# Performance work log

Hardware: AMD Instinct MI355X
Metric: run time of the kernel (lower is better)

Reference implementation:

```python
import jax, jax.numpy as jnp
import numpy as np

TAU = 0.05       # sinkhorn temperature (functools.partial in GCN_Net)
SK_ITERS = 20    # sinkhorn max_iter


def _mlp(x, w1, b1, w2, b2):
    # nn.Sequential(Linear, ReLU, Linear)
    return jnp.maximum(x @ w1 + b1, 0.0) @ w2 + b2


def _cosine(f1, f2, eps=1e-8):
    # torch CosineSimilarity over broadcast (E1,1,D) x (1,E2,D), computed as a GEMM
    n1 = jnp.maximum(jnp.linalg.norm(f1, axis=-1), eps)
    n2 = jnp.maximum(jnp.linalg.norm(f2, axis=-1), eps)
    return (f1 @ f2.T) / (n1[:, None] * n2[None, :])


def _sinkhorn(s):
    # log-domain sinkhorn, alternating row/col normalization (pygmtools-style)
    log_s = s / TAU
    for i in range(SK_ITERS):
        log_s = log_s - jax.nn.logsumexp(log_s, axis=(1 if i % 2 == 0 else 0), keepdims=True)
    return jnp.exp(log_s)


def _build_conn_edges(preds):
    # fully-connected off-diagonal graph; edge feats [dx, dy, dist, cls_src, cls_dst]
    n = preds.shape[0]
    pos = preds[:, 1:3]
    cls = preds[:, 6]
    idx = np.arange(n)
    r, c = np.meshgrid(idx, idx, indexing='ij')
    m = r != c
    conn = np.stack([r[m], c[m]], axis=1)  # (E,2), static under jit
    src, dst = conn[:, 0], conn[:, 1]
    d = pos[dst] - pos[src]                             # (E,2)
    dist = jnp.linalg.norm(d, axis=-1, keepdims=True)   # (E,1)
    edges = jnp.concatenate([d, dist, cls[src][:, None], cls[dst][:, None]], axis=-1)  # (E,5)
    return jnp.asarray(conn), edges


def _forward(ego_preds, cav_preds, node_w1, node_b1, node_w2, node_b2,
             edge_w1, edge_b1, edge_w2, edge_b2,
             l0_self_w, l0_self_b, l0_conv_w, l0_conv_b, l0_cls_w, l0_cls_b,
             l1_self_w, l1_self_b, l1_conv_w, l1_conv_b, l1_cls_w, l1_cls_b,
             fc_w, fc_b):
    ego = ego_preds[0]
    cav = cav_preds[0]
    n1, n2 = ego.shape[0], cav.shape[0]
    conn1, e1 = _build_conn_edges(ego)
    conn2, e2 = _build_conn_edges(cav)
    # --- NodeMLP affinity ---
    f1 = _mlp(ego[:, 1:6], node_w1, node_b1, node_w2, node_b2)
    f2 = _mlp(cav[:, 1:6], node_w1, node_b1, node_w2, node_b2)
    cls_eq = (ego[:, 6][:, None] == cav[:, 6][None, :]).astype(ego.dtype)
    conf = jnp.sum(jnp.sqrt(ego[:, 7:][:, None, :] * cav[:, 7:][None, :, :]), axis=-1)
    node_aff = cls_eq * conf * _cosine(f1, f2)                         # (n1,n2)
    # --- EdgeMLP affinity ---
    g1 = _mlp(e1[:, :3], edge_w1, edge_b1, edge_w2, edge_b2)
    g2 = _mlp(e2[:, :3], edge_w1, edge_b1, edge_w2, edge_b2)
    ecls = jnp.all(e1[:, 3:].astype(jnp.int32)[:, None, :] == e2[:, 3:].astype(jnp.int32)[None, :, :],
                   axis=-1).astype(ego.dtype)
    edge_aff = ecls * _cosine(g1, g2)                                  # (E1,E2)
    # --- Lawler affinity matrix K over association graph: node (i,a) -> i*n2+a ---
    N = n1 * n2
    rows = (conn1[:, 0][:, None] * n2 + conn2[:, 0][None, :]).ravel()
    cols = (conn1[:, 1][:, None] * n2 + conn2[:, 1][None, :]).ravel()
    K = jnp.zeros((N, N), ego.dtype).at[rows, cols].set(edge_aff.ravel())
    d_idx = jnp.arange(N)
    K = K.at[d_idx, d_idx].set(node_aff.ravel())
    # --- GCN adjacency = nonzero pattern of K, with added self-loops + sym norm ---
    A = (K != 0).astype(ego.dtype) + jnp.eye(N, dtype=ego.dtype)
    dinv = jax.lax.rsqrt(A.sum(axis=1))
    normA = dinv[:, None] * A * dinv[None, :]
    x = jnp.diag(K)[:, None]                                           # (N,1)
    # --- NGMConvLayers: self-loop Linear + GCNConv + sinkhorn channel ---
    for sw, sb, cw, cb, kw, kb in (
            (l0_self_w, l0_self_b, l0_conv_w, l0_conv_b, l0_cls_w, l0_cls_b),
            (l1_self_w, l1_self_b, l1_conv_w, l1_conv_b, l1_cls_w, l1_cls_b)):
        x = (x @ sw + sb) + (normA @ (x @ cw) + cb)
        sk = _sinkhorn((x @ kw + kb).reshape(n1, n2))
        x = x + sk.reshape(-1, 1)
    scores = x @ fc_w + fc_b                                           # (N,1)
    s = scores.reshape(n2, n1).T                                       # view(n2,-1).t()
    return _sinkhorn(s)


def setup_inputs() -> dict:
    key = jax.random.key(0)
    ks = jax.random.split(key, 16)

    def lin(k, fi, fo):
        kw, kb = jax.random.split(k)
        s = (2.0 / (fi + fo)) ** 0.5
        return (jax.random.normal(kw, (fi, fo), jnp.float32) * s,
                jax.random.normal(kb, (fo,), jnp.float32) * 0.01)

    def make_preds(k, n):
        k1, k2 = jax.random.split(k)
        p = jax.random.uniform(k1, (1, n, 8), jnp.float32)
        cls = jnp.floor(jax.random.uniform(k2, (1, n)) * 3.0)  # 3 discrete classes
        p = p.at[:, :, 6].set(cls)
        p = p.at[:, :, 7].set(0.1 + 0.9 * p[:, :, 7])          # positive confidences
        return p

    inp = {'ego_preds': make_preds(ks[0], 64), 'cav_preds': make_preds(ks[1], 64)}
    inp['node_w1'], inp['node_b1'] = lin(ks[2], 5, 64)
    inp['node_w2'], inp['node_b2'] = lin(ks[3], 64, 32)
    inp['edge_w1'], inp['edge_b1'] = lin(ks[4], 3, 64)
    inp['edge_w2'], inp['edge_b2'] = lin(ks[5], 64, 32)
    inp['l0_self_w'], inp['l0_self_b'] = lin(ks[6], 1, 16)
    inp['l0_conv_w'], inp['l0_conv_b'] = lin(ks[7], 1, 16)
    inp['l0_cls_w'], inp['l0_cls_b'] = lin(ks[8], 16, 1)
    inp['l1_self_w'], inp['l1_self_b'] = lin(ks[9], 16, 16)
    inp['l1_conv_w'], inp['l1_conv_b'] = lin(ks[10], 16, 16)
    inp['l1_cls_w'], inp['l1_cls_b'] = lin(ks[11], 16, 1)
    inp['fc_w'], inp['fc_b'] = lin(ks[12], 16, 1)
    return inp


def reference(ego_preds, cav_preds, node_w1, node_b1, node_w2, node_b2,
              edge_w1, edge_b1, edge_w2, edge_b2,
              l0_self_w, l0_self_b, l0_conv_w, l0_conv_b, l0_cls_w, l0_cls_b,
              l1_self_w, l1_self_b, l1_conv_w, l1_conv_b, l1_cls_w, l1_cls_b,
              fc_w, fc_b):
    return _forward(ego_preds, cav_preds, node_w1, node_b1, node_w2, node_b2,
                    edge_w1, edge_b1, edge_w2, edge_b2,
                    l0_self_w, l0_self_b, l0_conv_w, l0_conv_b, l0_cls_w, l0_cls_b,
                    l1_self_w, l1_self_b, l1_conv_w, l1_conv_b, l1_cls_w, l1_cls_b,
                    fc_w, fc_b)
```

## Files before the change

### kernel.cpp

```cpp
#include <hip/hip_runtime.h>
#include <math.h>


#define SK_SCALE 28.853900817779268f

template<int CTRL>
__device__ __forceinline__ float dppf(float x) {
    int xi = __float_as_int(x);
    int rr = __builtin_amdgcn_update_dpp(xi, xi, CTRL, 0xF, 0xF, false);
    return __int_as_float(rr);
}
__device__ __forceinline__ float red16_max(float v) {
    v = fmaxf(v, dppf<0xB1>(v));
    v = fmaxf(v, dppf<0x4E>(v));
    v = fmaxf(v, dppf<0x141>(v));
    v = fmaxf(v, dppf<0x140>(v));
    return v;
}
__device__ __forceinline__ float red16_sum(float v) {
    v += dppf<0xB1>(v); v += dppf<0x4E>(v); v += dppf<0x141>(v); v += dppf<0x140>(v);
    return v;
}
__device__ __forceinline__ float e2f(float x) { return __builtin_amdgcn_exp2f(x); }
__device__ __forceinline__ float rcpf(float x) { return __builtin_amdgcn_rcpf(x); }
__device__ __forceinline__ float dot4(const float4 a, const float4 b) {
    return a.x*b.x + a.y*b.y + a.z*b.z + a.w*b.w;
}
__device__ __forceinline__ void fma4(float4& a, float b, const float4 c) {
    a.x += b*c.x; a.y += b*c.y; a.z += b*c.z; a.w += b*c.w;
}
__device__ __forceinline__ void add4(float4& a, const float4 c) {
    a.x += c.x; a.y += c.y; a.z += c.z; a.w += c.w;
}
__device__ __forceinline__ void ld4(const float* p, float* o) {
    float4 v = *(const float4*)p; o[0]=v.x; o[1]=v.y; o[2]=v.z; o[3]=v.w;
}

__device__ void sk_mult(const float* tq, const float* tt, int s, int pr,
                        float* up, float* vp, float* rmp,
                        float* aq, float* att, float* u_out, float* v_out) {
    float rm = red16_max(fmaxf(fmaxf(tq[0], tq[1]), fmaxf(tq[2], tq[3])));
    #pragma unroll
    for (int k = 0; k < 4; ++k) aq[k] = e2f(tq[k] - rm);
    float u = rcpf(red16_sum(aq[0] + aq[1] + aq[2] + aq[3]));
    if (s == 0) { rmp[pr] = rm; up[pr] = u; }
    __syncthreads();
    float rmq[4]; ld4(rmp + 4*s, rmq);
    #pragma unroll
    for (int k = 0; k < 4; ++k) att[k] = e2f(tt[k] - rmq[k]);
    float v;
    {
        float uq[4]; ld4(up + 4*s, uq);
        v = rcpf(red16_sum(att[0]*uq[0] + att[1]*uq[1] + att[2]*uq[2] + att[3]*uq[3]));
        if (s == 0) vp[pr] = v;
        __syncthreads();
    }
    #pragma unroll 1
    for (int p = 0; p < 9; ++p) {
        float vq[4]; ld4(vp + 4*s, vq);
        u = rcpf(red16_sum(aq[0]*vq[0] + aq[1]*vq[1] + aq[2]*vq[2] + aq[3]*vq[3]));
        if (s == 0) up[pr] = u;
        __syncthreads();
        float uq[4]; ld4(up + 4*s, uq);
        v = rcpf(red16_sum(att[0]*uq[0] + att[1]*uq[1] + att[2]*uq[2] + att[3]*uq[3]));
        if (s == 0) vp[pr] = v;
        __syncthreads();
    }
    *u_out = u; *v_out = v;
}

__device__ void matvec_dual(const float* u1, const float* u1t, const float* u2, const float* u2t,
                            const float* mmq, const float* dqv, const float* mmt, const float* dqt,
                            float* o1, float* o1t, float* o2, float* o2t,
                            int s, int pr,
                            float* WR1p, float* WC1p, float* WR2p, float* WC2p) {
    float z1[4], z2[4], z1t[4], z2t[4];
    float rs1 = 0, rs2 = 0, cs1 = 0, cs2 = 0;
    #pragma unroll
    for (int k = 0; k < 4; ++k) {
        float md = mmq[k] * dqv[k], mdt = mmt[k] * dqt[k];
        z1[k] = md * u1[k];   z2[k] = md * u2[k];
        z1t[k] = mdt * u1t[k]; z2t[k] = mdt * u2t[k];
        rs1 += z1[k]; rs2 += z2[k]; cs1 += z1t[k]; cs2 += z2t[k];
    }
    rs1 = red16_sum(rs1); rs2 = red16_sum(rs2);
    cs1 = red16_sum(cs1); cs2 = red16_sum(cs2);
    if (s == 0) { WR1p[pr] = rs1; WR2p[pr] = rs2; WC1p[pr] = cs1; WC2p[pr] = cs2; }
    __syncthreads();
    float wr1[4], wc1[4], wr2[4], wc2[4];
    ld4(WR1p + 4*s, wr1); ld4(WC1p + 4*s, wc1);
    ld4(WR2p + 4*s, wr2); ld4(WC2p + 4*s, wc2);
    float W1 = red16_sum(wc1[0] + wc1[1] + wc1[2] + wc1[3]);
    float W2 = red16_sum(wc2[0] + wc2[1] + wc2[2] + wc2[3]);
    #pragma unroll
    for (int k = 0; k < 4; ++k) {
        float d = dqv[k], mm = mmq[k], dt = dqt[k], mt = mmt[k];
        o1[k]  = d  * ((1.0f + mm) * d  * u1[k]  + mm * (W1 - rs1 - wc1[k] + z1[k]));
        o2[k]  = d  * ((1.0f + mm) * d  * u2[k]  + mm * (W2 - rs2 - wc2[k] + z2[k]));
        o1t[k] = dt * ((1.0f + mt) * dt * u1t[k] + mt * (W1 - wr1[k] - cs1 + z1t[k]));
        o2t[k] = dt * ((1.0f + mt) * dt * u2t[k] + mt * (W2 - wr2[k] - cs2 + z2t[k]));
    }
}

extern "C" __global__ __launch_bounds__(1024)
void gcn_match_kernel(const float* ego, const float* cav,
                      const float* nw1, const float* nb1, const float* nw2, const float* nb2,
                      const float* sw0, const float* sb0, const float* cw0, const float* cb0,
                      const float* kw0, const float* kb0,
                      const float* sw1, const float* sb1, const float* cw1, const float* cb1,
                      const float* kw1, const float* kb1,
                      const float* fcw, const float* fcb,
                      float* out) {
    __shared__ __align__(16) float sh_hT1[64 * 68];
    __shared__ __align__(16) float sh_hT2[64 * 68];
    __shared__ __align__(16) float sh_w2[2048];
    __shared__ __align__(16) float sh_f1[64 * 36];
    __shared__ __align__(16) float sh_f2[64 * 36];
    __shared__ __align__(16) float sh_nb2[32];
    __shared__ float sh_cls1[64], sh_cf1[64], sh_n1[64];
    __shared__ __align__(16) float sh_cls1p[64], sh_cf1p[64], sh_n1p[64];
    __shared__ __align__(16) float sh_cls2p[64], sh_cf2p[64], sh_n2p[64];
    __shared__ __align__(16) float sh_Drp[64], sh_Dcp[64];
    __shared__ __align__(16) float sh_rmp[64], sh_up[64], sh_vp[64];
    __shared__ __align__(16) float sh_WR1p[64], sh_WC1p[64], sh_WR2p[64], sh_WC2p[64];
    __shared__ float sh_avec[7 * 16];
    __shared__ float sh_coef[18];

    const int tid  = threadIdx.x;
    const int wave = tid >> 6, lane = tid & 63;
    const int r = tid >> 4, s = tid & 15;
    const int pr = 4 * (r & 15) + (r >> 4);
    float* sh_dots = sh_hT1;

    if (tid < 512) ((float4*)sh_w2)[tid] = ((const float4*)nw2)[tid];
    if (tid < 32) sh_nb2[tid] = nb2[tid];
    if (tid < 64) {
        float c = ego[tid * 8 + 6], f = ego[tid * 8 + 7];
        int p = 4 * (tid & 15) + (tid >> 4);
        sh_cls1[tid] = c; sh_cf1[tid] = f; sh_cls1p[p] = c; sh_cf1p[p] = f;
    } else if (tid < 128) {
        int j = tid - 64, p = 4 * (j & 15) + (j >> 4);
        sh_cls2p[p] = cav[j * 8 + 6]; sh_cf2p[p] = cav[j * 8 + 7];
    }
    {
        const float* X = (wave < 8) ? ego : cav;
        float* HT = (wave < 8) ? sh_hT1 : sh_hT2;
        const int k0 = (wave & 7) * 8;
        float4 xa = ((const float4*)X)[lane * 2];
        float4 xb = ((const float4*)X)[lane * 2 + 1];
        #pragma unroll
        for (int kk = 0; kk < 8; ++kk) {
            int k = k0 + kk;
            float acc = nb1[k] + xa.y * nw1[k] + xa.z * nw1[64 + k] + xa.w * nw1[128 + k]
                      + xb.x * nw1[192 + k] + xb.y * nw1[256 + k];
            HT[k * 68 + lane] = fmaxf(acc, 0.0f);
        }
    }
    __syncthreads();

    if (wave < 2) {
        const float* HT = (wave == 0) ? sh_hT1 : sh_hT2;
        float* F = (wave == 0) ? sh_f1 : sh_f2;
        const int rr = lane >> 2, oq = lane & 3;
        float4 accA[4], accB[4];
        #pragma unroll
        for (int m = 0; m < 4; ++m) { accA[m] = make_float4(0,0,0,0); accB[m] = accA[m]; }
        #pragma unroll 4
        for (int k = 0; k < 64; ++k) {
            float4 hq = *(const float4*)(HT + k * 68 + 4 * rr);
            float4 wA = *(const float4*)(sh_w2 + k * 32 + 4 * oq);
            float4 wB = *(const float4*)(sh_w2 + k * 32 + 16 + 4 * oq);
            fma4(accA[0], hq.x, wA); fma4(accB[0], hq.x, wB);
            fma4(accA[1], hq.y, wA); fma4(accB[1], hq.y, wB);
            fma4(accA[2], hq.z, wA); fma4(accB[2], hq.z, wB);
            fma4(accA[3], hq.w, wA); fma4(accB[3], hq.w, wB);
        }
        float4 b2a = *(const float4*)(sh_nb2 + 4 * oq);
        float4 b2b = *(const float4*)(sh_nb2 + 16 + 4 * oq);
        float sq[4];
        #pragma unroll
        for (int m = 0; m < 4; ++m) {
            add4(accA[m], b2a); add4(accB[m], b2b);
            int row = 4 * rr + m;
            *(float4*)(F + row * 36 + 4 * oq)      = accA[m];
            *(float4*)(F + row * 36 + 16 + 4 * oq) = accB[m];
            float q = dot4(accA[m], accA[m]) + dot4(accB[m], accB[m]);
            q += dppf<0xB1>(q); q += dppf<0x4E>(q);
            sq[m] = q;
        }
        if (oq == 0) {
            #pragma unroll
            for (int m = 0; m < 4; ++m) {
                int row = 4 * rr + m, p = 4 * (row & 15) + (row >> 4);
                float n = fmaxf(sqrtf(sq[m]), 1e-8f);
                if (wave == 0) { sh_n1[row] = n; sh_n1p[p] = n; }
                else           { sh_n2p[p] = n; }
            }
        }
    } else if (wave == 2 && lane < 16) {
        int o = lane;
        float ax = 0, av = 0, as_ = 0, aw = 0, au = 0, ae = 0, a1 = 0;
        for (int k = 0; k < 16; ++k) {
            float s0k = sw0[k], c0k = cw0[k], b0k = sb0[k] + cb0[k];
            float s1ko = sw1[k * 16 + o], c1ko = cw1[k * 16 + o];
            ax += s0k * s1ko;  av += c0k * s1ko + s0k * c1ko;  as_ += s1ko;
            aw += c0k * c1ko;  au += c1ko;  ae += b0k * c1ko;  a1 += b0k * s1ko;
        }
        a1 += sb1[o] + cb1[o];
        sh_avec[0*16+o] = ax; sh_avec[1*16+o] = av; sh_avec[2*16+o] = as_;
        sh_avec[3*16+o] = aw; sh_avec[4*16+o] = au; sh_avec[5*16+o] = ae;
        sh_avec[6*16+o] = a1;
    }
    __syncthreads();

    if (wave < 4) {
        const int sc = lane & 15, rc = lane >> 4;
        float dt[4][4];
        #pragma unroll
        for (int m = 0; m < 4; ++m)
            #pragma unroll
            for (int k = 0; k < 4; ++k) dt[m][k] = 0.0f;
        for (int kq = 0; kq < 8; ++kq) {
            float4 f2q[4];
            #pragma unroll
            for (int k = 0; k < 4; ++k)
                f2q[k] = *(const float4*)(sh_f2 + (sc + 16 * k) * 36 + 4 * kq);
            #pragma unroll
            for (int m = 0; m < 4; ++m) {
                int rrow = 16 * m + 4 * wave + rc;
                float4 f1q = *(const float4*)(sh_f1 + rrow * 36 + 4 * kq);
                #pragma unroll
                for (int k = 0; k < 4; ++k) dt[m][k] += dot4(f1q, f2q[k]);
            }
        }
        #pragma unroll
        for (int m = 0; m < 4; ++m) {
            int rrow = 16 * m + 4 * wave + rc;
            *(float4*)(sh_dots + rrow * 68 + 4 * sc) =
                make_float4(dt[m][0], dt[m][1], dt[m][2], dt[m][3]);
        }
    } else if (wave == 4 && lane < 18) {
        int t = lane; float c = 0.0f;
        if (t == 0)      { for (int k = 0; k < 16; ++k) c += sw0[k] * kw0[k]; }
        else if (t == 1) { for (int k = 0; k < 16; ++k) c += cw0[k] * kw0[k]; }
        else if (t == 2) { for (int k = 0; k < 16; ++k) c += (sb0[k] + cb0[k]) * kw0[k]; c += kb0[0]; }
        else if (t < 10) { int v = t - 3;
            for (int o = 0; o < 16; ++o) c += sh_avec[v * 16 + o] * kw1[o];
            if (v == 6) c += kb1[0];
        } else if (t < 17) { int v = t - 10;
            for (int o = 0; o < 16; ++o) c += sh_avec[v * 16 + o] * fcw[o];
            if (v == 6) c += fcb[0];
        } else { for (int o = 0; o < 16; ++o) c += fcw[o]; }
        sh_coef[t] = c;
    }
    float mmq[4], mmt[4], cfq[4], cft[4];
    float Drr, Dcr;
    {
        const float cls1r = sh_cls1[r], cls2r = sh_cls2p[pr];
        const float cf1r = sh_cf1[r],  cf2r  = sh_cf2p[pr];
        float c2q[4], c1q[4], f2q[4], f1q[4];
        ld4(sh_cls2p + 4*s, c2q); ld4(sh_cls1p + 4*s, c1q);
        ld4(sh_cf2p + 4*s, f2q);  ld4(sh_cf1p + 4*s, f1q);
        float dr = 0, dc = 0;
        #pragma unroll
        for (int k = 0; k < 4; ++k) {
            mmq[k] = (cls1r == c2q[k]) ? 1.0f : 0.0f;
            mmt[k] = (c1q[k] == cls2r) ? 1.0f : 0.0f;
            dr += mmq[k]; dc += mmt[k];
            cfq[k] = sqrtf(cf1r * f2q[k]);
            cft[k] = sqrtf(f1q[k] * cf2r);
        }
        Drr = red16_sum(dr);
        Dcr = red16_sum(dc);
        if (s == 0) { sh_Drp[pr] = Drr; sh_Dcp[pr] = Dcr; }
    }
    __syncthreads();

    float dqv[4], dqt[4], x0[4], x0t[4];
    {
        float dcq[4], drq[4], n2q[4], n1q[4], dotq[4];
        ld4(sh_Dcp + 4*s, dcq); ld4(sh_Drp + 4*s, drq);
        ld4(sh_n2p + 4*s, n2q); ld4(sh_n1p + 4*s, n1q);
        ld4(sh_dots + r * 68 + 4*s, dotq);
        float Tdeg = red16_sum(dcq[0] + dcq[1] + dcq[2] + dcq[3]);
        const float n1r = sh_n1[r], n2r = sh_n2p[pr];
        #pragma unroll
        for (int k = 0; k < 4; ++k) {
            dqv[k] = (mmq[k] != 0.0f) ? (1.0f / sqrtf(Tdeg - Drr - dcq[k] + 3.0f)) : 1.0f;
            dqt[k] = (mmt[k] != 0.0f) ? (1.0f / sqrtf(Tdeg - drq[k] - Dcr + 3.0f)) : 1.0f;
            x0[k] = mmq[k] * cfq[k] * (dotq[k] / (n1r * n2q[k]));
            float dott = sh_dots[(s + 16 * k) * 68 + pr];
            x0t[k] = mmt[k] * cft[k] * (dott / (n1q[k] * n2r));
        }
    }

    float v0[4], v0t[4], oe[4], oet[4];
    {
        float ones[4] = {1.0f, 1.0f, 1.0f, 1.0f};
        matvec_dual(x0, x0t, ones, ones, mmq, dqv, mmt, dqt,
                    v0, v0t, oe, oet, s, pr, sh_WR1p, sh_WC1p, sh_WR2p, sh_WC2p);
    }

    float aq[4], att[4], u0, vv0;
    float s0[4], s0t[4];
    {
        float c0 = sh_coef[0], c1 = sh_coef[1], c2 = sh_coef[2];
        float t0q[4], t0t[4];
        #pragma unroll
        for (int k = 0; k < 4; ++k) {
            t0q[k] = (c0 * x0[k]  + c1 * v0[k]  + c2) * SK_SCALE;
            t0t[k] = (c0 * x0t[k] + c1 * v0t[k] + c2) * SK_SCALE;
        }
        sk_mult(t0q, t0t, s, pr, sh_up, sh_vp, sh_rmp, aq, att, &u0, &vv0);
        float vq[4], uq[4];
        ld4(sh_vp + 4*s, vq); ld4(sh_up + 4*s, uq);
        #pragma unroll
        for (int k = 0; k < 4; ++k) {
            s0[k]  = aq[k] * u0 * vq[k];
            s0t[k] = att[k] * uq[k] * vv0;
        }
    }

    float ov[4], ovt[4], os[4], ost[4];
    matvec_dual(v0, v0t, s0, s0t, mmq, dqv, mmt, dqt,
                ov, ovt, os, ost, s, pr, sh_WR1p, sh_WC1p, sh_WR2p, sh_WC2p);
    float t1q[4], t1t[4], sacc[4], sacct[4];
    {
        float ctx = sh_coef[3], ctv = sh_coef[4], cts = sh_coef[5];
        float cw_ = sh_coef[6], cu_ = sh_coef[7], ce_ = sh_coef[8], ct1 = sh_coef[9];
        float csx = sh_coef[10], csv = sh_coef[11], css = sh_coef[12];
        float cw2 = sh_coef[13], cu2 = sh_coef[14], ce2 = sh_coef[15], cs1 = sh_coef[16];
        #pragma unroll
        for (int k = 0; k < 4; ++k) {
            t1q[k] = (ctx * x0[k] + ctv * v0[k] + cts * s0[k] + ct1
                    + cw_ * ov[k] + cu_ * os[k] + ce_ * oe[k]) * SK_SCALE;
            t1t[k] = (ctx * x0t[k] + ctv * v0t[k] + cts * s0t[k] + ct1
                    + cw_ * ovt[k] + cu_ * ost[k] + ce_ * oet[k]) * SK_SCALE;
            sacc[k] = csx * x0[k] + csv * v0[k] + css * s0[k] + cs1
                    + cw2 * ov[k] + cu2 * os[k] + ce2 * oe[k];
            sacct[k] = csx * x0t[k] + csv * v0t[k] + css * s0t[k] + cs1
                    + cw2 * ovt[k] + cu2 * ost[k] + ce2 * oet[k];
        }
    }

    {
        float u1, v1;
        sk_mult(t1q, t1t, s, pr, sh_up, sh_vp, sh_rmp, aq, att, &u1, &v1);
        float c17 = sh_coef[17];
        float vq[4], uq[4];
        ld4(sh_vp + 4*s, vq); ld4(sh_up + 4*s, uq);
        #pragma unroll
        for (int k = 0; k < 4; ++k) {
            sacc[k]  += c17 * aq[k] * u1 * vq[k];
            sacct[k] += c17 * att[k] * uq[k] * v1;
        }
    }
    __syncthreads();

    {
        float t2q[4], t2t[4];
        #pragma unroll
        for (int k = 0; k < 4; ++k) {
            t2q[k] = sacct[k] * SK_SCALE;
            t2t[k] = sacc[k] * SK_SCALE;
        }
        float u2, v2;
        sk_mult(t2q, t2t, s, pr, sh_up, sh_vp, sh_rmp, aq, att, &u2, &v2);
        float vq[4]; ld4(sh_vp + 4*s, vq);
        #pragma unroll
        for (int k = 0; k < 4; ++k)
            out[(r << 6) + s + (k << 4)] = aq[k] * u2 * vq[k];
    }
}

extern "C" void kernel_launch(void* const* d_in, const int* in_sizes, int n_in,
                              void* d_out, int out_size, void* d_ws, size_t ws_size,
                              hipStream_t stream) {
    const float* ego = (const float*)d_in[0];
    const float* cav = (const float*)d_in[1];
    const float* nw1 = (const float*)d_in[2];
    const float* nb1 = (const float*)d_in[3];
    const float* nw2 = (const float*)d_in[4];
    const float* nb2 = (const float*)d_in[5];
    const float* sw0 = (const float*)d_in[10];
    const float* sb0 = (const float*)d_in[11];
    const float* cw0 = (const float*)d_in[12];
    const float* cb0 = (const float*)d_in[13];
    const float* kw0 = (const float*)d_in[14];
    const float* kb0 = (const float*)d_in[15];
    const float* sw1 = (const float*)d_in[16];
    const float* sb1 = (const float*)d_in[17];
    const float* cw1 = (const float*)d_in[18];
    const float* cb1 = (const float*)d_in[19];
    const float* kw1 = (const float*)d_in[20];
    const float* kb1 = (const float*)d_in[21];
    const float* fcw = (const float*)d_in[22];
    const float* fcb = (const float*)d_in[23];

    gcn_match_kernel<<<dim3(1), dim3(1024), 0, stream>>>(
        ego, cav, nw1, nb1, nw2, nb2,
        sw0, sb0, cw0, cb0, kw0, kb0,
        sw1, sb1, cw1, cb1, kw1, kb1,
        fcw, fcb, (float*)d_out);
}
```

Measured before the change: 123.9 us.

## Shrink block to 256 threads with 16 elements per thread and quad reductions

Reworks the single-block kernel from 1024 threads (16-lane groups, 4 elements each) to 256 threads where each group of 4 lanes owns a row and each lane holds 16 elements. Row and column reductions become 2-step quad DPP reductions plus serial in-register sums, which cuts cross-lane traffic and barrier cost across the many Sinkhorn iterations. It also stages all small weights in shared memory up front and hoists the Sinkhorn-independent terms out of the later combination. The trade-off is more serial work per thread and higher register pressure from the 16-wide arrays, so this latency-bound single-block kernel gives up thread-level parallelism.

```diff
diff --git a/kernel.cpp b/kernel.cpp
--- a/kernel.cpp
+++ b/kernel.cpp
@@ -10,16 +10,11 @@
     int rr = __builtin_amdgcn_update_dpp(xi, xi, CTRL, 0xF, 0xF, false);
     return __int_as_float(rr);
 }
-__device__ __forceinline__ float red16_max(float v) {
-    v = fmaxf(v, dppf<0xB1>(v));
-    v = fmaxf(v, dppf<0x4E>(v));
-    v = fmaxf(v, dppf<0x141>(v));
-    v = fmaxf(v, dppf<0x140>(v));
-    return v;
-}
-__device__ __forceinline__ float red16_sum(float v) {
-    v += dppf<0xB1>(v); v += dppf<0x4E>(v); v += dppf<0x141>(v); v += dppf<0x140>(v);
-    return v;
+__device__ __forceinline__ float quad_sum(float v) {
+    v += dppf<0xB1>(v); v += dppf<0x4E>(v); return v;
+}
+__device__ __forceinline__ float quad_max(float v) {
+    v = fmaxf(v, dppf<0xB1>(v)); v = fmaxf(v, dppf<0x4E>(v)); return v;
 }
 __device__ __forceinline__ float e2f(float x) { return __builtin_amdgcn_exp2f(x); }
 __device__ __forceinline__ float rcpf(float x) { return __builtin_amdgcn_rcpf(x); }
@@ -32,77 +27,106 @@
 __device__ __forceinline__ void add4(float4& a, const float4 c) {
     a.x += c.x; a.y += c.y; a.z += c.z; a.w += c.w;
 }
-__device__ __forceinline__ void ld4(const float* p, float* o) {
-    float4 v = *(const float4*)p; o[0]=v.x; o[1]=v.y; o[2]=v.z; o[3]=v.w;
-}
-
-__device__ void sk_mult(const float* tq, const float* tt, int s, int pr,
-                        float* up, float* vp, float* rmp,
-                        float* aq, float* att, float* u_out, float* v_out) {
-    float rm = red16_max(fmaxf(fmaxf(tq[0], tq[1]), fmaxf(tq[2], tq[3])));
-    #pragma unroll
-    for (int k = 0; k < 4; ++k) aq[k] = e2f(tq[k] - rm);
-    float u = rcpf(red16_sum(aq[0] + aq[1] + aq[2] + aq[3]));
-    if (s == 0) { rmp[pr] = rm; up[pr] = u; }
-    __syncthreads();
-    float rmq[4]; ld4(rmp + 4*s, rmq);
-    #pragma unroll
-    for (int k = 0; k < 4; ++k) att[k] = e2f(tt[k] - rmq[k]);
+__device__ __forceinline__ void ld16(const float* p, float* o) {
+    #pragma unroll
+    for (int t = 0; t < 4; ++t) {
+        float4 v = *(const float4*)(p + 4*t);
+        o[4*t+0]=v.x; o[4*t+1]=v.y; o[4*t+2]=v.z; o[4*t+3]=v.w;
+    }
+}
+__device__ __forceinline__ float dotsum16(const float* a, const float* b) {
+    float s0=0,s1=0,s2=0,s3=0;
+    #pragma unroll
+    for (int t = 0; t < 4; ++t) {
+        s0 += a[4*t+0]*b[4*t+0]; s1 += a[4*t+1]*b[4*t+1];
+        s2 += a[4*t+2]*b[4*t+2]; s3 += a[4*t+3]*b[4*t+3];
+    }
+    return (s0+s1)+(s2+s3);
+}
+__device__ __forceinline__ float sum16(const float* a) {
+    float s0=0,s1=0,s2=0,s3=0;
+    #pragma unroll
+    for (int t = 0; t < 4; ++t) {
+        s0 += a[4*t+0]; s1 += a[4*t+1]; s2 += a[4*t+2]; s3 += a[4*t+3];
+    }
+    return (s0+s1)+(s2+s3);
+}
+
+__device__ __forceinline__ void sk_mult(const float* tq, const float* tt, int q, int r,
+                                        float* up, float* vp, float* rmp,
+                                        float* aq, float* att, float* u_out, float* v_out) {
+    float rm = tq[0];
+    #pragma unroll
+    for (int m = 1; m < 16; ++m) rm = fmaxf(rm, tq[m]);
+    rm = quad_max(rm);
+    #pragma unroll
+    for (int m = 0; m < 16; ++m) aq[m] = e2f(tq[m] - rm);
+    float u = rcpf(quad_sum(sum16(aq)));
+    if (q == 0) { rmp[r] = rm; up[r] = u; }
+    __syncthreads();
+    float rmq[16]; ld16(rmp + 16*q, rmq);
+    #pragma unroll
+    for (int m = 0; m < 16; ++m) att[m] = e2f(tt[m] - rmq[m]);
     float v;
     {
-        float uq[4]; ld4(up + 4*s, uq);
-        v = rcpf(red16_sum(att[0]*uq[0] + att[1]*uq[1] + att[2]*uq[2] + att[3]*uq[3]));
-        if (s == 0) vp[pr] = v;
+        float uq[16]; ld16(up + 16*q, uq);
+        v = rcpf(quad_sum(dotsum16(att, uq)));
+        if (q == 0) vp[r] = v;
         __syncthreads();
     }
     #pragma unroll 1
     for (int p = 0; p < 9; ++p) {
-        float vq[4]; ld4(vp + 4*s, vq);
-        u = rcpf(red16_sum(aq[0]*vq[0] + aq[1]*vq[1] + aq[2]*vq[2] + aq[3]*vq[3]));
-        if (s == 0) up[pr] = u;
+        float vq[16]; ld16(vp + 16*q, vq);
+        u = rcpf(quad_sum(dotsum16(aq, vq)));
+        if (q == 0) up[r] = u;
         __syncthreads();
-        float uq[4]; ld4(up + 4*s, uq);
-        v = rcpf(red16_sum(att[0]*uq[0] + att[1]*uq[1] + att[2]*uq[2] + att[3]*uq[3]));
-        if (s == 0) vp[pr] = v;
+        float uq[16]; ld16(up + 16*q, uq);
+        v = rcpf(quad_sum(dotsum16(att, uq)));
+        if (q == 0) vp[r] = v;
         __syncthreads();
     }
     *u_out = u; *v_out = v;
 }
 
-__device__ void matvec_dual(const float* u1, const float* u1t, const float* u2, const float* u2t,
-                            const float* mmq, const float* dqv, const float* mmt, const float* dqt,
-                            float* o1, float* o1t, float* o2, float* o2t,
-                            int s, int pr,
-                            float* WR1p, float* WC1p, float* WR2p, float* WC2p) {
-    float z1[4], z2[4], z1t[4], z2t[4];
-    float rs1 = 0, rs2 = 0, cs1 = 0, cs2 = 0;
-    #pragma unroll
-    for (int k = 0; k < 4; ++k) {
-        float md = mmq[k] * dqv[k], mdt = mmt[k] * dqt[k];
-        z1[k] = md * u1[k];   z2[k] = md * u2[k];
-        z1t[k] = mdt * u1t[k]; z2t[k] = mdt * u2t[k];
-        rs1 += z1[k]; rs2 += z2[k]; cs1 += z1t[k]; cs2 += z2t[k];
-    }
-    rs1 = red16_sum(rs1); rs2 = red16_sum(rs2);
-    cs1 = red16_sum(cs1); cs2 = red16_sum(cs2);
-    if (s == 0) { WR1p[pr] = rs1; WR2p[pr] = rs2; WC1p[pr] = cs1; WC2p[pr] = cs2; }
-    __syncthreads();
-    float wr1[4], wc1[4], wr2[4], wc2[4];
-    ld4(WR1p + 4*s, wr1); ld4(WC1p + 4*s, wc1);
-    ld4(WR2p + 4*s, wr2); ld4(WC2p + 4*s, wc2);
-    float W1 = red16_sum(wc1[0] + wc1[1] + wc1[2] + wc1[3]);
-    float W2 = red16_sum(wc2[0] + wc2[1] + wc2[2] + wc2[3]);
-    #pragma unroll
-    for (int k = 0; k < 4; ++k) {
-        float d = dqv[k], mm = mmq[k], dt = dqt[k], mt = mmt[k];
-        o1[k]  = d  * ((1.0f + mm) * d  * u1[k]  + mm * (W1 - rs1 - wc1[k] + z1[k]));
-        o2[k]  = d  * ((1.0f + mm) * d  * u2[k]  + mm * (W2 - rs2 - wc2[k] + z2[k]));
-        o1t[k] = dt * ((1.0f + mt) * dt * u1t[k] + mt * (W1 - wr1[k] - cs1 + z1t[k]));
-        o2t[k] = dt * ((1.0f + mt) * dt * u2t[k] + mt * (W2 - wr2[k] - cs2 + z2t[k]));
-    }
-}
-
-extern "C" __global__ __launch_bounds__(1024)
+__device__ __forceinline__ void matvec_dual(const float* u1, const float* u1t,
+                                            const float* u2, const float* u2t,
+                                            const float* mmq, const float* dqv,
+                                            const float* mmt, const float* dqt,
+                                            float* o1, float* o1t, float* o2, float* o2t,
+                                            int q, int r,
+                                            float* WR1, float* WC1, float* WR2, float* WC2) {
+    float rs1=0, rs2=0, cs1=0, cs2=0;
+    #pragma unroll
+    for (int m = 0; m < 16; ++m) {
+        float md = mmq[m]*dqv[m], mdt = mmt[m]*dqt[m];
+        rs1 += md * u1[m];               cs1 += mdt * u1t[m];
+        rs2 += md * (u2 ? u2[m] : 1.0f); cs2 += mdt * (u2t ? u2t[m] : 1.0f);
+    }
+    rs1 = quad_sum(rs1); rs2 = quad_sum(rs2);
+    cs1 = quad_sum(cs1); cs2 = quad_sum(cs2);
+    if (q == 0) { WR1[r]=rs1; WR2[r]=rs2; WC1[r]=cs1; WC2[r]=cs2; }
+    __syncthreads();
+    float wr1[16], wc1[16], wr2[16], wc2[16];
+    ld16(WR1 + 16*q, wr1); ld16(WC1 + 16*q, wc1);
+    ld16(WR2 + 16*q, wr2); ld16(WC2 + 16*q, wc2);
+    float W1 = quad_sum(sum16(wc1));
+    float W2 = quad_sum(sum16(wc2));
+    #pragma unroll
+    for (int m = 0; m < 16; ++m) {
+        float d = dqv[m], mm = mmq[m];
+        float u1m = u1[m], u2m = u2 ? u2[m] : 1.0f;
+        float z1 = mm*d*u1m, z2 = mm*d*u2m;
+        o1[m] = d*((1.0f+mm)*d*u1m + mm*(W1 - rs1 - wc1[m] + z1));
+        o2[m] = d*((1.0f+mm)*d*u2m + mm*(W2 - rs2 - wc2[m] + z2));
+        float dt = dqt[m], mt = mmt[m];
+        float u1tm = u1t[m], u2tm = u2t ? u2t[m] : 1.0f;
+        float z1t = mt*dt*u1tm, z2t = mt*dt*u2tm;
+        o1t[m] = dt*((1.0f+mt)*dt*u1tm + mt*(W1 - wr1[m] - cs1 + z1t));
+        o2t[m] = dt*((1.0f+mt)*dt*u2tm + mt*(W2 - wr2[m] - cs2 + z2t));
+    }
+}
+
+extern "C" __global__ __launch_bounds__(256, 1)
 void gcn_match_kernel(const float* ego, const float* cav,
                       const float* nw1, const float* nb1, const float* nw2, const float* nb2,
                       const float* sw0, const float* sb0, const float* cw0, const float* cb0,
@@ -116,104 +140,132 @@
     __shared__ __align__(16) float sh_w2[2048];
     __shared__ __align__(16) float sh_f1[64 * 36];
     __shared__ __align__(16) float sh_f2[64 * 36];
-    __shared__ __align__(16) float sh_nb2[32];
-    __shared__ float sh_cls1[64], sh_cf1[64], sh_n1[64];
-    __shared__ __align__(16) float sh_cls1p[64], sh_cf1p[64], sh_n1p[64];
-    __shared__ __align__(16) float sh_cls2p[64], sh_cf2p[64], sh_n2p[64];
-    __shared__ __align__(16) float sh_Drp[64], sh_Dcp[64];
-    __shared__ __align__(16) float sh_rmp[64], sh_up[64], sh_vp[64];
-    __shared__ __align__(16) float sh_WR1p[64], sh_WC1p[64], sh_WR2p[64], sh_WC2p[64];
+    __shared__ __align__(16) float sh_nw1[320];
+    __shared__ __align__(16) float sh_nb1[64], sh_nb2[32];
+    __shared__ __align__(16) float sh_cls1[64], sh_cf1[64], sh_cls2[64], sh_cf2[64];
+    __shared__ __align__(16) float sh_n1[64], sh_n2[64], sh_Dr[64], sh_Dc[64];
+    __shared__ __align__(16) float sh_up[64], sh_vp[64], sh_rmp[64];
+    __shared__ __align__(16) float sh_WR1[64], sh_WC1[64], sh_WR2[64], sh_WC2[64];
+    __shared__ __align__(16) float sh_sw0[16], sh_sb0[16], sh_cw0[16], sh_cb0[16];
+    __shared__ __align__(16) float sh_sb1[16], sh_cb1[16];
+    __shared__ __align__(16) float sh_sw1[256], sh_cw1[256];
+    __shared__ __align__(16) float sh_kw0[16], sh_kw1[16], sh_fcw[16];
+    __shared__ float sh_kb[4];
     __shared__ float sh_avec[7 * 16];
     __shared__ float sh_coef[18];
 
-    const int tid  = threadIdx.x;
-    const int wave = tid >> 6, lane = tid & 63;
-    const int r = tid >> 4, s = tid & 15;
-    const int pr = 4 * (r & 15) + (r >> 4);
-    float* sh_dots = sh_hT1;
-
-    if (tid < 512) ((float4*)sh_w2)[tid] = ((const float4*)nw2)[tid];
-    if (tid < 32) sh_nb2[tid] = nb2[tid];
-    if (tid < 64) {
-        float c = ego[tid * 8 + 6], f = ego[tid * 8 + 7];
-        int p = 4 * (tid & 15) + (tid >> 4);
-        sh_cls1[tid] = c; sh_cf1[tid] = f; sh_cls1p[p] = c; sh_cf1p[p] = f;
-    } else if (tid < 128) {
-        int j = tid - 64, p = 4 * (j & 15) + (j >> 4);
-        sh_cls2p[p] = cav[j * 8 + 6]; sh_cf2p[p] = cav[j * 8 + 7];
-    }
-    {
-        const float* X = (wave < 8) ? ego : cav;
-        float* HT = (wave < 8) ? sh_hT1 : sh_hT2;
-        const int k0 = (wave & 7) * 8;
-        float4 xa = ((const float4*)X)[lane * 2];
-        float4 xb = ((const float4*)X)[lane * 2 + 1];
-        #pragma unroll
-        for (int kk = 0; kk < 8; ++kk) {
-            int k = k0 + kk;
-            float acc = nb1[k] + xa.y * nw1[k] + xa.z * nw1[64 + k] + xa.w * nw1[128 + k]
-                      + xb.x * nw1[192 + k] + xb.y * nw1[256 + k];
-            HT[k * 68 + lane] = fmaxf(acc, 0.0f);
-        }
-    }
-    __syncthreads();
-
-    if (wave < 2) {
-        const float* HT = (wave == 0) ? sh_hT1 : sh_hT2;
-        float* F = (wave == 0) ? sh_f1 : sh_f2;
+    const int tid = threadIdx.x;
+    const int wv = tid >> 6, lane = tid & 63;
+    const int r = tid >> 2, q = tid & 3;
+
+    ((float4*)sh_w2)[tid]       = ((const float4*)nw2)[tid];
+    ((float4*)sh_w2)[tid + 256] = ((const float4*)nw2)[tid + 256];
+    if (tid < 80)       ((float4*)sh_nw1)[tid]      = ((const float4*)nw1)[tid];
+    else if (tid < 96)  ((float4*)sh_nb1)[tid-80]   = ((const float4*)nb1)[tid-80];
+    else if (tid < 104) ((float4*)sh_nb2)[tid-96]   = ((const float4*)nb2)[tid-96];
+    else if (tid < 108) ((float4*)sh_sw0)[tid-104]  = ((const float4*)sw0)[tid-104];
+    else if (tid < 112) ((float4*)sh_sb0)[tid-108]  = ((const float4*)sb0)[tid-108];
+    else if (tid < 116) ((float4*)sh_cw0)[tid-112]  = ((const float4*)cw0)[tid-112];
+    else if (tid < 120) ((float4*)sh_cb0)[tid-116]  = ((const float4*)cb0)[tid-116];
+    else if (tid < 124) ((float4*)sh_sb1)[tid-120]  = ((const float4*)sb1)[tid-120];
+    else if (tid < 128) ((float4*)sh_cb1)[tid-124]  = ((const float4*)cb1)[tid-124];
+    else if (tid < 192) ((float4*)sh_sw1)[tid-128]  = ((const float4*)sw1)[tid-128];
+    else                ((float4*)sh_cw1)[tid-192]  = ((const float4*)cw1)[tid-192];
+    if (tid < 4)        ((float4*)sh_kw0)[tid]      = ((const float4*)kw0)[tid];
+    else if (tid < 8)   ((float4*)sh_kw1)[tid-4]    = ((const float4*)kw1)[tid-4];
+    else if (tid < 12)  ((float4*)sh_fcw)[tid-8]    = ((const float4*)fcw)[tid-8];
+    else if (tid == 12) sh_kb[0] = kb0[0];
+    else if (tid == 13) sh_kb[1] = kb1[0];
+    else if (tid == 14) sh_kb[2] = fcb[0];
+    if (tid < 64) { sh_cls1[tid] = ego[tid*8+6]; sh_cf1[tid] = ego[tid*8+7]; }
+    else if (tid < 128) { int j = tid-64; sh_cls2[j] = cav[j*8+6]; sh_cf2[j] = cav[j*8+7]; }
+    __syncthreads();
+
+    {
+        float4 ea = ((const float4*)ego)[lane*2], eb = ((const float4*)ego)[lane*2+1];
+        float4 ca = ((const float4*)cav)[lane*2], cb = ((const float4*)cav)[lane*2+1];
+        #pragma unroll
+        for (int kk = 0; kk < 16; ++kk) {
+            int k = 16*wv + kk;
+            float b1 = sh_nb1[k];
+            float w0 = sh_nw1[k],       w1 = sh_nw1[64+k],  w2_ = sh_nw1[128+k];
+            float w3 = sh_nw1[192+k],   w4 = sh_nw1[256+k];
+            sh_hT1[k*68 + lane] = fmaxf(b1 + ea.y*w0 + ea.z*w1 + ea.w*w2_ + eb.x*w3 + eb.y*w4, 0.0f);
+            sh_hT2[k*68 + lane] = fmaxf(b1 + ca.y*w0 + ca.z*w1 + ca.w*w2_ + cb.x*w3 + cb.y*w4, 0.0f);
+        }
+    }
+    __syncthreads();
+
+    if (wv < 2) {
+        const float* HT = (wv == 0) ? sh_hT1 : sh_hT2;
+        float* F  = (wv == 0) ? sh_f1 : sh_f2;
+        float* NN = (wv == 0) ? sh_n1 : sh_n2;
         const int rr = lane >> 2, oq = lane & 3;
         float4 accA[4], accB[4];
         #pragma unroll
         for (int m = 0; m < 4; ++m) { accA[m] = make_float4(0,0,0,0); accB[m] = accA[m]; }
         #pragma unroll 4
         for (int k = 0; k < 64; ++k) {
-            float4 hq = *(const float4*)(HT + k * 68 + 4 * rr);
-            float4 wA = *(const float4*)(sh_w2 + k * 32 + 4 * oq);
-            float4 wB = *(const float4*)(sh_w2 + k * 32 + 16 + 4 * oq);
+            float4 hq = *(const float4*)(HT + k*68 + 4*rr);
+            float4 wA = *(const float4*)(sh_w2 + k*32 + 4*oq);
+            float4 wB = *(const float4*)(sh_w2 + k*32 + 16 + 4*oq);
             fma4(accA[0], hq.x, wA); fma4(accB[0], hq.x, wB);
             fma4(accA[1], hq.y, wA); fma4(accB[1], hq.y, wB);
             fma4(accA[2], hq.z, wA); fma4(accB[2], hq.z, wB);
             fma4(accA[3], hq.w, wA); fma4(accB[3], hq.w, wB);
         }
-        float4 b2a = *(const float4*)(sh_nb2 + 4 * oq);
-        float4 b2b = *(const float4*)(sh_nb2 + 16 + 4 * oq);
+        float4 b2a = *(const float4*)(sh_nb2 + 4*oq);
+        float4 b2b = *(const float4*)(sh_nb2 + 16 + 4*oq);
         float sq[4];
         #pragma unroll
         for (int m = 0; m < 4; ++m) {
             add4(accA[m], b2a); add4(accB[m], b2b);
-            int row = 4 * rr + m;
-            *(float4*)(F + row * 36 + 4 * oq)      = accA[m];
-            *(float4*)(F + row * 36 + 16 + 4 * oq) = accB[m];
-            float q = dot4(accA[m], accA[m]) + dot4(accB[m], accB[m]);
-            q += dppf<0xB1>(q); q += dppf<0x4E>(q);
-            sq[m] = q;
+            int row = 4*rr + m;
+            *(float4*)(F + row*36 + 4*oq)      = accA[m];
+            *(float4*)(F + row*36 + 16 + 4*oq) = accB[m];
+            float q2 = dot4(accA[m], accA[m]) + dot4(accB[m], accB[m]);
+            q2 += dppf<0xB1>(q2); q2 += dppf<0x4E>(q2);
+            sq[m] = q2;
         }
         if (oq == 0) {
             #pragma unroll
-            for (int m = 0; m < 4; ++m) {
-                int row = 4 * rr + m, p = 4 * (row & 15) + (row >> 4);
-                float n = fmaxf(sqrtf(sq[m]), 1e-8f);
-                if (wave == 0) { sh_n1[row] = n; sh_n1p[p] = n; }
-                else           { sh_n2p[p] = n; }
+            for (int m = 0; m < 4; ++m)
+                NN[4*rr + m] = fmaxf(sqrtf(sq[m]), 1e-8f);
+        }
+    } else if (wv == 2) {
+        if (lane < 16) {
+            int o = lane;
+            float ax=0, av=0, as_=0, aw=0, au=0, ae=0, a1=0;
+            #pragma unroll
+            for (int k = 0; k < 16; ++k) {
+                float s0k = sh_sw0[k], c0k = sh_cw0[k], b0k = sh_sb0[k] + sh_cb0[k];
+                float s1ko = sh_sw1[k*16+o], c1ko = sh_cw1[k*16+o];
+                ax += s0k*s1ko;  av += c0k*s1ko + s0k*c1ko;  as_ += s1ko;
+                aw += c0k*c1ko;  au += c1ko;  ae += b0k*c1ko;  a1 += b0k*s1ko;
             }
-        }
-    } else if (wave == 2 && lane < 16) {
-        int o = lane;
-        float ax = 0, av = 0, as_ = 0, aw = 0, au = 0, ae = 0, a1 = 0;
-        for (int k = 0; k < 16; ++k) {
-            float s0k = sw0[k], c0k = cw0[k], b0k = sb0[k] + cb0[k];
-            float s1ko = sw1[k * 16 + o], c1ko = cw1[k * 16 + o];
-            ax += s0k * s1ko;  av += c0k * s1ko + s0k * c1ko;  as_ += s1ko;
-            aw += c0k * c1ko;  au += c1ko;  ae += b0k * c1ko;  a1 += b0k * s1ko;
-        }
-        a1 += sb1[o] + cb1[o];
-        sh_avec[0*16+o] = ax; sh_avec[1*16+o] = av; sh_avec[2*16+o] = as_;
-        sh_avec[3*16+o] = aw; sh_avec[4*16+o] = au; sh_avec[5*16+o] = ae;
-        sh_avec[6*16+o] = a1;
-    }
-    __syncthreads();
-
-    if (wave < 4) {
+            a1 += sh_sb1[o] + sh_cb1[o];
+            sh_avec[0*16+o]=ax; sh_avec[1*16+o]=av; sh_avec[2*16+o]=as_;
+            sh_avec[3*16+o]=aw; sh_avec[4*16+o]=au; sh_avec[5*16+o]=ae;
+            sh_avec[6*16+o]=a1;
+        }
+        if (lane < 18) {
+            int t = lane; float c = 0.0f;
+            if (t == 0)      { for (int k = 0; k < 16; ++k) c += sh_sw0[k]*sh_kw0[k]; }
+            else if (t == 1) { for (int k = 0; k < 16; ++k) c += sh_cw0[k]*sh_kw0[k]; }
+            else if (t == 2) { for (int k = 0; k < 16; ++k) c += (sh_sb0[k]+sh_cb0[k])*sh_kw0[k]; c += sh_kb[0]; }
+            else if (t < 10) { int v = t-3;
+                for (int o = 0; o < 16; ++o) c += sh_avec[v*16+o]*sh_kw1[o];
+                if (v == 6) c += sh_kb[1];
+            } else if (t < 17) { int v = t-10;
+                for (int o = 0; o < 16; ++o) c += sh_avec[v*16+o]*sh_fcw[o];
+                if (v == 6) c += sh_kb[2];
+            } else { for (int o = 0; o < 16; ++o) c += sh_fcw[o]; }
+            sh_coef[t] = c;
+        }
+    }
+    __syncthreads();
+
+    {
         const int sc = lane & 15, rc = lane >> 4;
         float dt[4][4];
         #pragma unroll
@@ -224,152 +276,148 @@
             float4 f2q[4];
             #pragma unroll
             for (int k = 0; k < 4; ++k)
-                f2q[k] = *(const float4*)(sh_f2 + (sc + 16 * k) * 36 + 4 * kq);
+                f2q[k] = *(const float4*)(sh_f2 + (sc + 16*k)*36 + 4*kq);
             #pragma unroll
             for (int m = 0; m < 4; ++m) {
-                int rrow = 16 * m + 4 * wave + rc;
-                float4 f1q = *(const float4*)(sh_f1 + rrow * 36 + 4 * kq);
+                int rrow = 16*m + 4*wv + rc;
+                float4 f1q = *(const float4*)(sh_f1 + rrow*36 + 4*kq);
                 #pragma unroll
                 for (int k = 0; k < 4; ++k) dt[m][k] += dot4(f1q, f2q[k]);
             }
         }
         #pragma unroll
         for (int m = 0; m < 4; ++m) {
-            int rrow = 16 * m + 4 * wave + rc;
-            *(float4*)(sh_dots + rrow * 68 + 4 * sc) =
-                make_float4(dt[m][0], dt[m][1], dt[m][2], dt[m][3]);
-        }
-    } else if (wave == 4 && lane < 18) {
-        int t = lane; float c = 0.0f;
-        if (t == 0)      { for (int k = 0; k < 16; ++k) c += sw0[k] * kw0[k]; }
-        else if (t == 1) { for (int k = 0; k < 16; ++k) c += cw0[k] * kw0[k]; }
-        else if (t == 2) { for (int k = 0; k < 16; ++k) c += (sb0[k] + cb0[k]) * kw0[k]; c += kb0[0]; }
-        else if (t < 10) { int v = t - 3;
-            for (int o = 0; o < 16; ++o) c += sh_avec[v * 16 + o] * kw1[o];
-            if (v == 6) c += kb1[0];
-        } else if (t < 17) { int v = t - 10;
-            for (int o = 0; o < 16; ++o) c += sh_avec[v * 16 + o] * fcw[o];
-            if (v == 6) c += fcb[0];
-        } else { for (int o = 0; o < 16; ++o) c += fcw[o]; }
-        sh_coef[t] = c;
-    }
-    float mmq[4], mmt[4], cfq[4], cft[4];
+            int rrow = 16*m + 4*wv + rc;
+            #pragma unroll
+            for (int k = 0; k < 4; ++k) {
+                sh_hT1[rrow*68 + sc + 16*k] = dt[m][k];
+                sh_hT2[(sc + 16*k)*68 + rrow] = dt[m][k];
+            }
+        }
+    }
+    float mmq[16], mmt[16], cfq[16], cft[16];
     float Drr, Dcr;
     {
-        const float cls1r = sh_cls1[r], cls2r = sh_cls2p[pr];
-        const float cf1r = sh_cf1[r],  cf2r  = sh_cf2p[pr];
-        float c2q[4], c1q[4], f2q[4], f1q[4];
-        ld4(sh_cls2p + 4*s, c2q); ld4(sh_cls1p + 4*s, c1q);
-        ld4(sh_cf2p + 4*s, f2q);  ld4(sh_cf1p + 4*s, f1q);
+        float c2q[16], c1q[16], f2v[16], f1v[16];
+        ld16(sh_cls2 + 16*q, c2q); ld16(sh_cls1 + 16*q, c1q);
+        ld16(sh_cf2 + 16*q, f2v);  ld16(sh_cf1 + 16*q, f1v);
+        const float cls1r = sh_cls1[r], cls2r = sh_cls2[r];
+        const float cf1r = sh_cf1[r],  cf2r  = sh_cf2[r];
         float dr = 0, dc = 0;
         #pragma unroll
-        for (int k = 0; k < 4; ++k) {
-            mmq[k] = (cls1r == c2q[k]) ? 1.0f : 0.0f;
-            mmt[k] = (c1q[k] == cls2r) ? 1.0f : 0.0f;
-            dr += mmq[k]; dc += mmt[k];
-            cfq[k] = sqrtf(cf1r * f2q[k]);
-            cft[k] = sqrtf(f1q[k] * cf2r);
-        }
-        Drr = red16_sum(dr);
-        Dcr = red16_sum(dc);
-        if (s == 0) { sh_Drp[pr] = Drr; sh_Dcp[pr] = Dcr; }
-    }
-    __syncthreads();
-
-    float dqv[4], dqt[4], x0[4], x0t[4];
-    {
-        float dcq[4], drq[4], n2q[4], n1q[4], dotq[4];
-        ld4(sh_Dcp + 4*s, dcq); ld4(sh_Drp + 4*s, drq);
-        ld4(sh_n2p + 4*s, n2q); ld4(sh_n1p + 4*s, n1q);
-        ld4(sh_dots + r * 68 + 4*s, dotq);
-        float Tdeg = red16_sum(dcq[0] + dcq[1] + dcq[2] + dcq[3]);
-        const float n1r = sh_n1[r], n2r = sh_n2p[pr];
-        #pragma unroll
-        for (int k = 0; k < 4; ++k) {
-            dqv[k] = (mmq[k] != 0.0f) ? (1.0f / sqrtf(Tdeg - Drr - dcq[k] + 3.0f)) : 1.0f;
-            dqt[k] = (mmt[k] != 0.0f) ? (1.0f / sqrtf(Tdeg - drq[k] - Dcr + 3.0f)) : 1.0f;
-            x0[k] = mmq[k] * cfq[k] * (dotq[k] / (n1r * n2q[k]));
-            float dott = sh_dots[(s + 16 * k) * 68 + pr];
-            x0t[k] = mmt[k] * cft[k] * (dott / (n1q[k] * n2r));
-        }
-    }
-
-    float v0[4], v0t[4], oe[4], oet[4];
-    {
-        float ones[4] = {1.0f, 1.0f, 1.0f, 1.0f};
-        matvec_dual(x0, x0t, ones, ones, mmq, dqv, mmt, dqt,
-                    v0, v0t, oe, oet, s, pr, sh_WR1p, sh_WC1p, sh_WR2p, sh_WC2p);
-    }
-
-    float aq[4], att[4], u0, vv0;
-    float s0[4], s0t[4];
+        for (int m = 0; m < 16; ++m) {
+            mmq[m] = (cls1r == c2q[m]) ? 1.0f : 0.0f;
+            mmt[m] = (c1q[m] == cls2r) ? 1.0f : 0.0f;
+            dr += mmq[m]; dc += mmt[m];
+            cfq[m] = sqrtf(cf1r * f2v[m]);
+            cft[m] = sqrtf(f1v[m] * cf2r);
+        }
+        Drr = quad_sum(dr);
+        Dcr = quad_sum(dc);
+        if (q == 0) { sh_Dr[r] = Drr; sh_Dc[r] = Dcr; }
+    }
+    __syncthreads();
+
+    float dqv[16], dqt[16], x0[16], x0t[16];
+    {
+        float dcq[16], drq[16], n2q[16], n1q[16], dotq[16], dotTq[16];
+        ld16(sh_Dc + 16*q, dcq); ld16(sh_Dr + 16*q, drq);
+        ld16(sh_n2 + 16*q, n2q); ld16(sh_n1 + 16*q, n1q);
+        ld16(sh_hT1 + r*68 + 16*q, dotq);
+        ld16(sh_hT2 + r*68 + 16*q, dotTq);
+        float Tdeg = quad_sum(sum16(dcq));
+        const float n1r = sh_n1[r], n2r = sh_n2[r];
+        #pragma unroll
+        for (int m = 0; m < 16; ++m) {
+            dqv[m] = (mmq[m] != 0.0f) ? (1.0f / sqrtf(Tdeg - Drr - dcq[m] + 3.0f)) : 1.0f;
+            dqt[m] = (mmt[m] != 0.0f) ? (1.0f / sqrtf(Tdeg - drq[m] - Dcr + 3.0f)) : 1.0f;
+            x0[m]  = mmq[m] * cfq[m] * (dotq[m]  / (n1r * n2q[m]));
+            x0t[m] = mmt[m] * cft[m] * (dotTq[m] / (n1q[m] * n2r));
+        }
+    }
+
+    float v0[16], v0t[16], oe[16], oet[16];
+    matvec_dual(x0, x0t, nullptr, nullptr, mmq, dqv, mmt, dqt,
+                v0, v0t, oe, oet, q, r, sh_WR1, sh_WC1, sh_WR2, sh_WC2);
+
+    float t0q[16], t0t[16], t1b[16], t1bt[16], sbse[16], sbst[16];
     {
         float c0 = sh_coef[0], c1 = sh_coef[1], c2 = sh_coef[2];
-        float t0q[4], t0t[4];
-        #pragma unroll
-        for (int k = 0; k < 4; ++k) {
-            t0q[k] = (c0 * x0[k]  + c1 * v0[k]  + c2) * SK_SCALE;
-            t0t[k] = (c0 * x0t[k] + c1 * v0t[k] + c2) * SK_SCALE;
-        }
-        sk_mult(t0q, t0t, s, pr, sh_up, sh_vp, sh_rmp, aq, att, &u0, &vv0);
-        float vq[4], uq[4];
-        ld4(sh_vp + 4*s, vq); ld4(sh_up + 4*s, uq);
-        #pragma unroll
-        for (int k = 0; k < 4; ++k) {
-            s0[k]  = aq[k] * u0 * vq[k];
-            s0t[k] = att[k] * uq[k] * vv0;
-        }
-    }
-
-    float ov[4], ovt[4], os[4], ost[4];
-    matvec_dual(v0, v0t, s0, s0t, mmq, dqv, mmt, dqt,
-                ov, ovt, os, ost, s, pr, sh_WR1p, sh_WC1p, sh_WR2p, sh_WC2p);
-    float t1q[4], t1t[4], sacc[4], sacct[4];
-    {
-        float ctx = sh_coef[3], ctv = sh_coef[4], cts = sh_coef[5];
-        float cw_ = sh_coef[6], cu_ = sh_coef[7], ce_ = sh_coef[8], ct1 = sh_coef[9];
-        float csx = sh_coef[10], csv = sh_coef[11], css = sh_coef[12];
-        float cw2 = sh_coef[13], cu2 = sh_coef[14], ce2 = sh_coef[15], cs1 = sh_coef[16];
-        #pragma unroll
-        for (int k = 0; k < 4; ++k) {
-            t1q[k] = (ctx * x0[k] + ctv * v0[k] + cts * s0[k] + ct1
-                    + cw_ * ov[k] + cu_ * os[k] + ce_ * oe[k]) * SK_SCALE;
-            t1t[k] = (ctx * x0t[k] + ctv * v0t[k] + cts * s0t[k] + ct1
-                    + cw_ * ovt[k] + cu_ * ost[k] + ce_ * oet[k]) * SK_SCALE;
-            sacc[k] = csx * x0[k] + csv * v0[k] + css * s0[k] + cs1
-                    + cw2 * ov[k] + cu2 * os[k] + ce2 * oe[k];
-            sacct[k] = csx * x0t[k] + csv * v0t[k] + css * s0t[k] + cs1
-                    + cw2 * ovt[k] + cu2 * ost[k] + ce2 * oet[k];
-        }
-    }
-
-    {
-        float u1, v1;
-        sk_mult(t1q, t1t, s, pr, sh_up, sh_vp, sh_rmp, aq, att, &u1, &v1);
+        float ctx = sh_coef[3], ctv = sh_coef[4];
+        float ce_ = sh_coef[8], ct1 = sh_coef[9];
+        float csx = sh_coef[10], csv = sh_coef[11];
+        float ce2 = sh_coef[15], cs1 = sh_coef[16];
+        #pragma unroll
+        for (int m = 0; m < 16; ++m) {
+            t0q[m] = (c0*x0[m]  + c1*v0[m]  + c2) * SK_SCALE;
+            t0t[m] = (c0*x0t[m] + c1*v0t[m] + c2) * SK_SCALE;
+            t1b[m]  = ctx*x0[m]  + ctv*v0[m]  + ct1 + ce_*oe[m];
+            t1bt[m] = ctx*x0t[m] + ctv*v0t[m] + ct1 + ce_*oet[m];
+            sbse[m] = csx*x0[m]  + csv*v0[m]  + cs1 + ce2*oe[m];
+            sbst[m] = csx*x0t[m] + csv*v0t[m] + cs1 + ce2*oet[m];
+        }
+    }
+
+    float aq[16], att[16], u_, v_;
+    sk_mult(t0q, t0t, q, r, sh_up, sh_vp, sh_rmp, aq, att, &u_, &v_);
+    float s0v[16], s0t[16];
+    {
+        float vq[16], uq[16];
+        ld16(sh_vp + 16*q, vq); ld16(sh_up + 16*q, uq);
+        #pragma unroll
+        for (int m = 0; m < 16; ++m) {
+            s0v[m] = aq[m] * u_ * vq[m];
+            s0t[m] = att[m] * uq[m] * v_;
+        }
+    }
+
+    float ov[16], ovt[16], os[16], ost[16];
+    matvec_dual(v0, v0t, s0v, s0t, mmq, dqv, mmt, dqt,
+                ov, ovt, os, ost, q, r, sh_WR1, sh_WC1, sh_WR2, sh_WC2);
+    float t1q[16], t1t[16], sacc[16], sacct[16];
+    {
+        float cts = sh_coef[5], cw_ = sh_coef[6], cu_ = sh_coef[7];
+        float css = sh_coef[12], cw2 = sh_coef[13], cu2 = sh_coef[14];
+        #pragma unroll
+        for (int m = 0; m < 16; ++m) {
+            t1q[m] = (t1b[m]  + cts*s0v[m] + cw_*ov[m]  + cu_*os[m])  * SK_SCALE;
+            t1t[m] = (t1bt[m] + cts*s0t[m] + cw_*ovt[m] + cu_*ost[m]) * SK_SCALE;
+            sacc[m]  = sbse[m] + css*s0v[m] + cw2*ov[m]  + cu2*os[m];
+            sacct[m] = sbst[m] + css*s0t[m] + cw2*ovt[m] + cu2*ost[m];
+        }
+    }
+
+    sk_mult(t1q, t1t, q, r, sh_up, sh_vp, sh_rmp, aq, att, &u_, &v_);
+    {
         float c17 = sh_coef[17];
-        float vq[4], uq[4];
-        ld4(sh_vp + 4*s, vq); ld4(sh_up + 4*s, uq);
-        #pragma unroll
-        for (int k = 0; k < 4; ++k) {
-            sacc[k]  += c17 * aq[k] * u1 * vq[k];
-            sacct[k] += c17 * att[k] * uq[k] * v1;
-        }
-    }
-    __syncthreads();
-
-    {
-        float t2q[4], t2t[4];
-        #pragma unroll
-        for (int k = 0; k < 4; ++k) {
-            t2q[k] = sacct[k] * SK_SCALE;
-            t2t[k] = sacc[k] * SK_SCALE;
-        }
-        float u2, v2;
-        sk_mult(t2q, t2t, s, pr, sh_up, sh_vp, sh_rmp, aq, att, &u2, &v2);
-        float vq[4]; ld4(sh_vp + 4*s, vq);
-        #pragma unroll
-        for (int k = 0; k < 4; ++k)
-            out[(r << 6) + s + (k << 4)] = aq[k] * u2 * vq[k];
+        float vq[16], uq[16];
+        ld16(sh_vp + 16*q, vq); ld16(sh_up + 16*q, uq);
+        #pragma unroll
+        for (int m = 0; m < 16; ++m) {
+            sacc[m]  += c17 * aq[m] * u_ * vq[m];
+            sacct[m] += c17 * att[m] * uq[m] * v_;
+        }
+    }
+    __syncthreads();
+
+    {
+        float t2q[16], t2t[16];
+        #pragma unroll
+        for (int m = 0; m < 16; ++m) {
+            t2q[m] = sacct[m] * SK_SCALE;
+            t2t[m] = sacc[m] * SK_SCALE;
+        }
+        sk_mult(t2q, t2t, q, r, sh_up, sh_vp, sh_rmp, aq, att, &u_, &v_);
+        float vq[16]; ld16(sh_vp + 16*q, vq);
+        #pragma unroll
+        for (int t = 0; t < 4; ++t) {
+            float4 o4;
+            o4.x = aq[4*t+0] * u_ * vq[4*t+0];
+            o4.y = aq[4*t+1] * u_ * vq[4*t+1];
+            o4.z = aq[4*t+2] * u_ * vq[4*t+2];
+            o4.w = aq[4*t+3] * u_ * vq[4*t+3];
+            *(float4*)(out + r*64 + 16*q + 4*t) = o4;
+        }
     }
 }
 
@@ -397,7 +445,7 @@
     const float* fcw = (const float*)d_in[22];
     const float* fcb = (const float*)d_in[23];
 
-    gcn_match_kernel<<<dim3(1), dim3(1024), 0, stream>>>(
+    gcn_match_kernel<<<dim3(1), dim3(256), 0, stream>>>(
         ego, cav, nw1, nb1, nw2, nb2,
         sw0, sb0, cw0, cb0, kw0, kb0,
         sw1, sb1, cw1, cb1, kw1, kb1,
```

Measured after the change: 124.3 us, median of 2. Within noise of the previous version (+0.3%).
